# Kernel optimization log

Hardware: AMD Instinct MI355X
Metric: run time of the kernel (lower is better)

The kernel has to match this reference:

```python
import jax, jax.numpy as jnp
import numpy as np

N, E, IN_F, EDGE_F, HID, S = 200000, 600000, 28, 4, 128, 20000
NUM_LAYERS = 4
L = NUM_LAYERS - 1
BN_EPS = 1e-5


def setup_inputs() -> dict:
    key = jax.random.key(0)
    ks = jax.random.split(key, 20)
    p = lambda k, shape: (jax.random.normal(k, shape, dtype=jnp.float32) * 0.1)
    return {
        'x': jax.random.normal(ks[0], (N, IN_F), dtype=jnp.float32),
        'edge_index': jax.random.randint(ks[1], (2, E), 0, N),
        'edge_attr': jax.random.normal(ks[2], (E, EDGE_F), dtype=jnp.float32),
        'edge_weight': jax.random.uniform(ks[3], (E,), dtype=jnp.float32),
        'node_mask': (jax.random.uniform(ks[4], (N,)) > 0.5).astype(jnp.float32),
        'subgraphs2nodes': jax.random.randint(ks[5], (N,), 0, S),
        # layer-1 params (in_features -> hidden)
        'be1_W1': p(ks[6], (EDGE_F, IN_F)), 'be1_b1': jnp.zeros((IN_F,), jnp.float32),
        'be1_W2': p(ks[7], (IN_F, IN_F)), 'be1_b2': jnp.zeros((IN_F,), jnp.float32),
        'm1_W1': p(ks[8], (IN_F, HID)), 'm1_b1': jnp.zeros((HID,), jnp.float32),
        'm1_W2': p(ks[9], (HID, HID)), 'm1_b2': jnp.zeros((HID,), jnp.float32),
        'bn1_g': jnp.ones((HID,), jnp.float32), 'bn1_b': jnp.zeros((HID,), jnp.float32),
        'eps1': jnp.zeros((), jnp.float32),
        # layers 2..NUM_LAYERS, stacked (hidden -> hidden)
        'beW1': p(ks[10], (L, EDGE_F, HID)), 'beb1': jnp.zeros((L, HID), jnp.float32),
        'beW2': p(ks[11], (L, HID, HID)), 'beb2': jnp.zeros((L, HID), jnp.float32),
        'mW1': p(ks[12], (L, HID, HID)), 'mb1': jnp.zeros((L, HID), jnp.float32),
        'mW2': p(ks[13], (L, HID, HID)), 'mb2': jnp.zeros((L, HID), jnp.float32),
        'bng': jnp.ones((L, HID), jnp.float32), 'bnb': jnp.zeros((L, HID), jnp.float32),
        'eps': jnp.zeros((L,), jnp.float32),
    }


def _mlp2(h, W1, b1, W2, b2):
    # Linear -> ReLU -> Linear
    return jnp.dot(jax.nn.relu(jnp.dot(h, W1) + b1), W2) + b2


def _gine(x, src, dst, edge_attr, edge_weight, eps,
          beW1, beb1, beW2, beb2, W1, b1, W2, b2, g, beta):
    # bond encoder on edge features
    e = _mlp2(edge_attr, beW1, beb1, beW2, beb2)            # [E, d]
    # message: relu(x_j + e_ij) * w_ij, aggregated at dst via scatter-add
    m = jax.nn.relu(x[src] + e) * edge_weight[:, None]      # [E, d]
    aggr = jax.ops.segment_sum(m, dst, num_segments=N)      # [N, d]
    h = (1.0 + eps) * x + aggr
    # node MLP: Linear,ReLU,Linear,BN(train mode),ReLU
    h = _mlp2(h, W1, b1, W2, b2)
    mu = jnp.mean(h, axis=0)
    var = jnp.mean((h - mu) ** 2, axis=0)
    h = (h - mu) * jax.lax.rsqrt(var + BN_EPS) * g + beta
    return jax.nn.relu(h)


def reference(x, edge_index, edge_attr, edge_weight, node_mask, subgraphs2nodes,
              be1_W1, be1_b1, be1_W2, be1_b2, m1_W1, m1_b1, m1_W2, m1_b2,
              bn1_g, bn1_b, eps1,
              beW1, beb1, beW2, beb2, mW1, mb1, mW2, mb2, bng, bnb, eps):
    src, dst = edge_index[0], edge_index[1]
    h = _gine(x, src, dst, edge_attr, edge_weight, eps1,
              be1_W1, be1_b1, be1_W2, be1_b2,
              m1_W1, m1_b1, m1_W2, m1_b2, bn1_g, bn1_b)
    for i in range(L):
        h_new = _gine(h, src, dst, edge_attr, edge_weight, eps[i],
                      beW1[i], beb1[i], beW2[i], beb2[i],
                      mW1[i], mb1[i], mW2[i], mb2[i], bng[i], bnb[i])
        h = h + h_new  # residual
    # float node_mask branch + global_add_pool over subgraphs2nodes
    h = h * node_mask[:, None]
    return jax.ops.segment_sum(h, subgraphs2nodes, num_segments=S)  # [S, HID]
```

## Files before the change

### kernel.cpp

```cpp
#include <hip/hip_runtime.h>
#include <hip/hip_bf16.h>


#define BNEPS 1e-5f
#define LDA 136
#define SCAN_NB 240

typedef __attribute__((ext_vector_type(8))) short bf16x8;
typedef __attribute__((ext_vector_type(8))) unsigned short u16x8;
typedef __attribute__((ext_vector_type(4))) float f32x4;

__device__ inline short f2bf(float f) {
    __hip_bfloat16 h = __float2bfloat16(f);
    return *reinterpret_cast<short*>(&h);
}
__device__ inline unsigned short f2bfu(float f) {
    __hip_bfloat16 h = __float2bfloat16(f);
    return *reinterpret_cast<unsigned short*>(&h);
}
__device__ inline float bf2f(unsigned short u) {
    union { unsigned int i; float f; } v; v.i = ((unsigned int)u) << 16; return v.f;
}

__global__ __launch_bounds__(256) void k_prep(
    const float* __restrict__ m1W2, const float* __restrict__ beW2,
    const float* __restrict__ mW1, const float* __restrict__ mW2,
    short* __restrict__ out)
{
    __shared__ float tileS[64][65];
    int b = blockIdx.x, mat = b >> 2, t = b & 3;
    const float* Wsrc;
    if (mat == 0) Wsrc = m1W2;
    else {
        int l = (mat - 1) / 3, which = (mat - 1) % 3;
        Wsrc = (which == 0) ? beW2 + (size_t)l * 16384
             : (which == 1) ? mW1 + (size_t)l * 16384
             :                mW2 + (size_t)l * 16384;
    }
    short* dst = out + (size_t)mat * 16384;
    int tr = (t >> 1) * 64, tc = (t & 1) * 64;
    for (int i = threadIdx.x; i < 4096; i += 256) {
        int r = i >> 6, c = i & 63;
        tileS[r][c] = Wsrc[(size_t)(tr + r) * 128 + (tc + c)];
    }
    __syncthreads();
    for (int i = threadIdx.x; i < 4096; i += 256) {
        int n = i >> 6, k = i & 63;
        dst[(size_t)(tc + n) * 128 + (tr + k)] = f2bf(tileS[k][n]);
    }
}

__global__ __launch_bounds__(256) void k_prep1(
    const float* __restrict__ W1, short* __restrict__ out)
{
    for (int i = threadIdx.x; i < 128 * 32; i += 256) {
        int n = i >> 5, k = i & 31;
        out[i] = (k < 28) ? f2bf(W1[(size_t)k * 128 + n]) : (short)0;
    }
}

__global__ __launch_bounds__(256) void k_prep28(
    const float* __restrict__ W2, short* __restrict__ out)
{
    for (int i = threadIdx.x; i < 32 * 32; i += 256) {
        int n = i >> 5, k = i & 31;
        out[i] = (n < 28 && k < 28) ? f2bf(W2[(size_t)k * 28 + n]) : (short)0;
    }
}

__global__ __launch_bounds__(256) void k_count(
    const int* __restrict__ ei, int* __restrict__ counts, int E)
{
    for (int e = blockIdx.x * 256 + threadIdx.x; e < E; e += gridDim.x * 256)
        atomicAdd(&counts[ei[E + e]], 1);
}

__global__ __launch_bounds__(256) void k_count2(
    const int* __restrict__ s2n, const float* __restrict__ mask,
    int* __restrict__ counts2, int N)
{
    for (int n = blockIdx.x * 256 + threadIdx.x; n < N; n += gridDim.x * 256)
        if (mask[n] != 0.f) atomicAdd(&counts2[s2n[n]], 1);
}

__global__ __launch_bounds__(256) void k_scanA(
    const int* __restrict__ counts, int* __restrict__ bsum, int N, int seg)
{
    __shared__ int red[256];
    int b = blockIdx.x;
    int lo = b * seg, hi = min(lo + seg, N);
    int s = 0;
    for (int i = lo + threadIdx.x; i < hi; i += 256) s += counts[i];
    red[threadIdx.x] = s;
    __syncthreads();
    for (int d = 128; d > 0; d >>= 1) {
        if (threadIdx.x < d) red[threadIdx.x] += red[threadIdx.x + d];
        __syncthreads();
    }
    if (threadIdx.x == 0) bsum[b] = red[0];
}

__global__ __launch_bounds__(256) void k_scanB(
    int* __restrict__ bsum, int nb, int* __restrict__ offs, int N)
{
    __shared__ int sh[256];
    int v = (threadIdx.x < nb) ? bsum[threadIdx.x] : 0;
    sh[threadIdx.x] = v;
    __syncthreads();
    for (int d = 1; d < 256; d <<= 1) {
        int t = (threadIdx.x >= d) ? sh[threadIdx.x - d] : 0;
        __syncthreads();
        sh[threadIdx.x] += t;
        __syncthreads();
    }
    if (threadIdx.x < nb) bsum[threadIdx.x] = sh[threadIdx.x] - v;
    if (threadIdx.x == 0) offs[N] = sh[255];
}

__global__ __launch_bounds__(256) void k_scanC(
    const int* __restrict__ counts, const int* __restrict__ bsum,
    int* __restrict__ offs, int* __restrict__ cursor, int N, int seg)
{
    __shared__ int sh[256];
    int b = blockIdx.x;
    int lo = b * seg, hi = min(lo + seg, N);
    int base = bsum[b];
    for (int t0 = lo; t0 < hi; t0 += 256) {
        int i = t0 + threadIdx.x;
        int v = (i < hi) ? counts[i] : 0;
        sh[threadIdx.x] = v;
        __syncthreads();
        for (int d = 1; d < 256; d <<= 1) {
            int t = (threadIdx.x >= d) ? sh[threadIdx.x - d] : 0;
            __syncthreads();
            sh[threadIdx.x] += t;
            __syncthreads();
        }
        int excl = base + sh[threadIdx.x] - v;
        if (i < hi) { offs[i] = excl; cursor[i] = excl; }
        int tileTotal = sh[255];
        __syncthreads();
        base += tileTotal;
    }
}

__global__ __launch_bounds__(256) void k_scatter(
    const int* __restrict__ ei, const float* __restrict__ ew,
    const float4* __restrict__ ea4,
    int* __restrict__ cursor, int2* __restrict__ pmeta,
    float4* __restrict__ pea4, int E)
{
    for (int e = blockIdx.x * 256 + threadIdx.x; e < E; e += gridDim.x * 256) {
        int d = ei[E + e];
        int pos = atomicAdd(&cursor[d], 1);
        pmeta[pos] = make_int2(ei[e], __float_as_int(ew[e]));
        pea4[pos] = ea4[e];
    }
}

__global__ __launch_bounds__(256) void k_scatter2(
    const int* __restrict__ s2n, const float* __restrict__ mask,
    int* __restrict__ cursor2, int* __restrict__ perm2, int N)
{
    for (int n = blockIdx.x * 256 + threadIdx.x; n < N; n += gridDim.x * 256)
        if (mask[n] != 0.f) {
            int pos = atomicAdd(&cursor2[s2n[n]], 1);
            perm2[pos] = n;
        }
}

__global__ __launch_bounds__(256) void k_emsg(
    const float4* __restrict__ pea4,
    const float* __restrict__ W1, const float* __restrict__ b1,
    const short* __restrict__ W2t, const float* __restrict__ b2,
    unsigned short* __restrict__ emsg, int e0, int e1)
{
    __shared__ short Bs[128 * LDA];
    __shared__ short As[64 * LDA];
    __shared__ float eas[64][4];
    int tid = threadIdx.x;
    for (int i = tid; i < 2048; i += 256) {
        int n = (i * 8) >> 7, k = (i * 8) & 127;
        *(bf16x8*)&Bs[n * LDA + k] = *(const bf16x8*)&W2t[i * 8];
    }
    int j = tid & 127, half = tid >> 7;
    float w10 = W1[j], w11 = W1[128 + j], w12 = W1[256 + j], w13 = W1[384 + j];
    float b1j = b1[j];
    int w = tid >> 6, lane = tid & 63;
    int l15 = lane & 15, quad = lane >> 4;
    __syncthreads();

    int numTiles = (e1 - e0 + 63) >> 6;
    for (int tile = blockIdx.x; tile < numTiles; tile += gridDim.x) {
        int base = e0 + tile * 64;
        __syncthreads();
        if (tid < 64) {
            int k = base + tid;
            float4 a = make_float4(0.f, 0.f, 0.f, 0.f);
            if (k < e1) a = pea4[k];
            eas[tid][0] = a.x; eas[tid][1] = a.y; eas[tid][2] = a.z; eas[tid][3] = a.w;
        }
        __syncthreads();
        #pragma unroll
        for (int q = 0; q < 32; ++q) {
            int e = half * 32 + q;
            float t = fmaf(eas[e][0], w10, fmaf(eas[e][1], w11,
                      fmaf(eas[e][2], w12, fmaf(eas[e][3], w13, b1j))));
            As[e * LDA + j] = f2bf(fmaxf(t, 0.f));
        }
        __syncthreads();
        f32x4 acc[8];
        #pragma unroll
        for (int nt = 0; nt < 8; ++nt) acc[nt] = (f32x4){0.f, 0.f, 0.f, 0.f};
        #pragma unroll
        for (int kt = 0; kt < 4; ++kt) {
            bf16x8 af = *(bf16x8*)&As[(w * 16 + l15) * LDA + kt * 32 + quad * 8];
            #pragma unroll
            for (int nt = 0; nt < 8; ++nt) {
                bf16x8 bf = *(bf16x8*)&Bs[(nt * 16 + l15) * LDA + kt * 32 + quad * 8];
                acc[nt] = __builtin_amdgcn_mfma_f32_16x16x32_bf16(af, bf, acc[nt], 0, 0, 0);
            }
        }
        #pragma unroll
        for (int nt = 0; nt < 8; ++nt) {
            int col = nt * 16 + l15;
            float b2c = b2[col];
            #pragma unroll
            for (int r = 0; r < 4; ++r) {
                int row = w * 16 + quad * 4 + r;
                As[row * LDA + col] = f2bf(acc[nt][r] + b2c);
            }
        }
        __syncthreads();
        #pragma unroll
        for (int kk = 0; kk < 4; ++kk) {
            int i = tid + kk * 256;
            int row = (i * 8) >> 7, col = (i * 8) & 127;
            int gr = base + row;
            if (gr < e1)
                *(bf16x8*)&emsg[(size_t)(gr - e0) * 128 + col] = *(bf16x8*)&As[row * LDA + col];
        }
    }
}

__global__ __launch_bounds__(256) void k_emsg28_mm(
    const float4* __restrict__ pea4,
    const float* __restrict__ W1, const float* __restrict__ b1,
    const short* __restrict__ W2t28,
    const float* __restrict__ b2,
    unsigned short* __restrict__ emsg28, int E)
{
    __shared__ short Bs[32 * 40];
    __shared__ short As[64 * 40];
    __shared__ float eas[64][4];
    __shared__ float b2s[32];
    int tid = threadIdx.x;
    for (int i = tid; i < 32 * 32; i += 256) {
        int n = i >> 5, k = i & 31;
        Bs[n * 40 + k] = W2t28[i];
    }
    if (tid < 32) b2s[tid] = (tid < 28) ? b2[tid] : 0.f;
    int j = tid & 31, sub = tid >> 5;
    float w10 = 0.f, w11 = 0.f, w12 = 0.f, w13 = 0.f, b1j = 0.f;
    if (j < 28) { w10 = W1[j]; w11 = W1[28 + j]; w12 = W1[56 + j]; w13 = W1[84 + j]; b1j = b1[j]; }
    int w = tid >> 6, lane = tid & 63;
    int l15 = lane & 15, quad = lane >> 4;
    __syncthreads();

    int numTiles = (E + 63) >> 6;
    for (int tile = blockIdx.x; tile < numTiles; tile += gridDim.x) {
        int base = tile * 64;
        __syncthreads();
        if (tid < 64) {
            int k = base + tid;
            float4 a = (k < E) ? pea4[k] : make_float4(0.f, 0.f, 0.f, 0.f);
            eas[tid][0] = a.x; eas[tid][1] = a.y; eas[tid][2] = a.z; eas[tid][3] = a.w;
        }
        __syncthreads();
        #pragma unroll
        for (int q = 0; q < 8; ++q) {
            int e = q * 8 + sub;
            float t = fmaf(eas[e][0], w10, fmaf(eas[e][1], w11,
                      fmaf(eas[e][2], w12, fmaf(eas[e][3], w13, b1j))));
            As[e * 40 + j] = (j < 28) ? f2bf(fmaxf(t, 0.f)) : (short)0;
        }
        __syncthreads();
        f32x4 acc[2];
        acc[0] = (f32x4){0.f, 0.f, 0.f, 0.f};
        acc[1] = (f32x4){0.f, 0.f, 0.f, 0.f};
        bf16x8 af = *(bf16x8*)&As[(w * 16 + l15) * 40 + quad * 8];
        #pragma unroll
        for (int nt = 0; nt < 2; ++nt) {
            bf16x8 bf = *(bf16x8*)&Bs[(nt * 16 + l15) * 40 + quad * 8];
            acc[nt] = __builtin_amdgcn_mfma_f32_16x16x32_bf16(af, bf, acc[nt], 0, 0, 0);
        }
        __syncthreads();
        #pragma unroll
        for (int nt = 0; nt < 2; ++nt) {
            int col = nt * 16 + l15;
            float bb = b2s[col];
            #pragma unroll
            for (int r = 0; r < 4; ++r)
                As[(w * 16 + quad * 4 + r) * 40 + col] = f2bf(acc[nt][r] + bb);
        }
        __syncthreads();
        for (int i = tid; i < 64 * 28; i += 256) {
            int row = i / 28, col = i - row * 28;
            int gr = base + row;
            if (gr < E) emsg28[(size_t)gr * 28 + col] = As[row * 40 + col];
        }
    }
}

__global__ __launch_bounds__(256) void k_gather(
    const unsigned short* __restrict__ h, const int* __restrict__ offs,
    const int2* __restrict__ pmeta, const unsigned short* __restrict__ emsg,
    unsigned short* __restrict__ a0,
    const float* __restrict__ epsp, int epsIdx, int init,
    int e0, int e1, int N)
{
    int grp = threadIdx.x >> 5, lane = threadIdx.x & 31;
    int n = blockIdx.x * 8 + grp;
    if (n >= N) return;
    int k0 = offs[n], k1 = offs[n + 1];
    int lo = max(k0, e0), hi = min(k1, e1);
    if (!init && lo >= hi) return;
    float m0 = 0.f, m1 = 0.f, m2 = 0.f, m3 = 0.f;
    for (int k = lo; k < hi; ++k) {
        int2 mt = pmeta[k];
        float w = __int_as_float(mt.y);
        ushort4 ev = *(const ushort4*)&emsg[(size_t)(k - e0) * 128 + lane * 4];
        ushort4 hv = *(const ushort4*)&h[(size_t)mt.x * 128 + lane * 4];
        m0 += fmaxf(bf2f(hv.x) + bf2f(ev.x), 0.f) * w;
        m1 += fmaxf(bf2f(hv.y) + bf2f(ev.y), 0.f) * w;
        m2 += fmaxf(bf2f(hv.z) + bf2f(ev.z), 0.f) * w;
        m3 += fmaxf(bf2f(hv.w) + bf2f(ev.w), 0.f) * w;
    }
    if (init) {
        float s = 1.0f + epsp[epsIdx];
        ushort4 hv = *(const ushort4*)&h[(size_t)n * 128 + lane * 4];
        m0 = fmaf(s, bf2f(hv.x), m0);
        m1 = fmaf(s, bf2f(hv.y), m1);
        m2 = fmaf(s, bf2f(hv.z), m2);
        m3 = fmaf(s, bf2f(hv.w), m3);
    } else {
        ushort4 cur = *(ushort4*)&a0[(size_t)n * 128 + lane * 4];
        m0 += bf2f(cur.x); m1 += bf2f(cur.y); m2 += bf2f(cur.z); m3 += bf2f(cur.w);
    }
    ushort4 o;
    o.x = f2bfu(m0); o.y = f2bfu(m1); o.z = f2bfu(m2); o.w = f2bfu(m3);
    *(ushort4*)&a0[(size_t)n * 128 + lane * 4] = o;
}

__global__ __launch_bounds__(256) void k_gather28(
    const float* __restrict__ x, const int* __restrict__ offs,
    const int2* __restrict__ pmeta, const unsigned short* __restrict__ emsg28,
    const float* __restrict__ eps1, float* __restrict__ u28, int N)
{
    int grp = threadIdx.x >> 5, lane = threadIdx.x & 31;
    int n = blockIdx.x * 8 + grp;
    if (n >= N || lane >= 28) return;
    float s = 1.0f + eps1[0];
    int k0 = offs[n], k1 = offs[n + 1];
    float m = 0.f;
    for (int k = k0; k < k1; ++k) {
        int2 mt = pmeta[k];
        float w = __int_as_float(mt.y);
        float e = bf2f(emsg28[(size_t)k * 28 + lane]);
        m += fmaxf(x[(size_t)mt.x * 28 + lane] + e, 0.f) * w;
    }
    u28[(size_t)n * 28 + lane] = fmaf(s, x[(size_t)n * 28 + lane], m);
}

__global__ __launch_bounds__(512) void k_mlp(
    const unsigned short* __restrict__ src, const short* __restrict__ Wt1,
    const float* __restrict__ b1, const short* __restrict__ Wt2,
    const float* __restrict__ b2, unsigned short* __restrict__ dst,
    float* __restrict__ stats, int N)
{
    __shared__ short Bs1[128 * LDA];
    __shared__ short Bs2[128 * LDA];
    __shared__ short As[128 * LDA];
    __shared__ float sstat[256];
    int tid = threadIdx.x;
    for (int i = tid; i < 2048; i += 512) {
        int n = (i * 8) >> 7, k = (i * 8) & 127;
        *(bf16x8*)&Bs1[n * LDA + k] = *(const bf16x8*)&Wt1[i * 8];
        *(bf16x8*)&Bs2[n * LDA + k] = *(const bf16x8*)&Wt2[i * 8];
    }
    if (tid < 256) sstat[tid] = 0.f;
    int w = tid >> 6, lane = tid & 63;
    int l15 = lane & 15, quad = lane >> 4;
    float b1r[8], b2r[8], lsum[8], lsq[8];
    #pragma unroll
    for (int nt = 0; nt < 8; ++nt) {
        int col = nt * 16 + l15;
        b1r[nt] = b1[col]; b2r[nt] = b2[col];
        lsum[nt] = 0.f; lsq[nt] = 0.f;
    }
    __syncthreads();

    int numTiles = (N + 127) >> 7;
    for (int tile = blockIdx.x; tile < numTiles; tile += gridDim.x) {
        int base = tile * 128;
        __syncthreads();
        #pragma unroll
        for (int kk = 0; kk < 4; ++kk) {
            int i = tid + kk * 512;
            int row = (i * 8) >> 7, col = (i * 8) & 127;
            int rr = base + row;
            bf16x8 v;
            if (rr < N) v = *(const bf16x8*)&src[(size_t)rr * 128 + col];
            else        v = (bf16x8){0,0,0,0,0,0,0,0};
            *(bf16x8*)&As[row * LDA + col] = v;
        }
        __syncthreads();
        f32x4 acc[8];
        #pragma unroll
        for (int nt = 0; nt < 8; ++nt) acc[nt] = (f32x4){0.f, 0.f, 0.f, 0.f};
        #pragma unroll
        for (int kt = 0; kt < 4; ++kt) {
            bf16x8 af = *(bf16x8*)&As[(w * 16 + l15) * LDA + kt * 32 + quad * 8];
            #pragma unroll
            for (int nt = 0; nt < 8; ++nt) {
                bf16x8 bf = *(bf16x8*)&Bs1[(nt * 16 + l15) * LDA + kt * 32 + quad * 8];
                acc[nt] = __builtin_amdgcn_mfma_f32_16x16x32_bf16(af, bf, acc[nt], 0, 0, 0);
            }
        }
        #pragma unroll
        for (int nt = 0; nt < 8; ++nt) {
            int col = nt * 16 + l15;
            #pragma unroll
            for (int r = 0; r < 4; ++r)
                As[(w * 16 + quad * 4 + r) * LDA + col] = f2bf(fmaxf(acc[nt][r] + b1r[nt], 0.f));
        }
        __syncthreads();
        #pragma unroll
        for (int nt = 0; nt < 8; ++nt) acc[nt] = (f32x4){0.f, 0.f, 0.f, 0.f};
        #pragma unroll
        for (int kt = 0; kt < 4; ++kt) {
            bf16x8 af = *(bf16x8*)&As[(w * 16 + l15) * LDA + kt * 32 + quad * 8];
            #pragma unroll
            for (int nt = 0; nt < 8; ++nt) {
                bf16x8 bf = *(bf16x8*)&Bs2[(nt * 16 + l15) * LDA + kt * 32 + quad * 8];
                acc[nt] = __builtin_amdgcn_mfma_f32_16x16x32_bf16(af, bf, acc[nt], 0, 0, 0);
            }
        }
        int row0 = base + w * 16 + quad * 4;
        #pragma unroll
        for (int nt = 0; nt < 8; ++nt) {
            int col = nt * 16 + l15;
            #pragma unroll
            for (int r = 0; r < 4; ++r) {
                float z = acc[nt][r] + b2r[nt];
                if (row0 + r < N) { lsum[nt] += z; lsq[nt] = fmaf(z, z, lsq[nt]); }
                As[(w * 16 + quad * 4 + r) * LDA + col] = f2bf(z);
            }
        }
        __syncthreads();
        #pragma unroll
        for (int kk = 0; kk < 4; ++kk) {
            int i = tid + kk * 512;
            int row = (i * 8) >> 7, col = (i * 8) & 127;
            int rr = base + row;
            if (rr < N)
                *(bf16x8*)&dst[(size_t)rr * 128 + col] = *(bf16x8*)&As[row * LDA + col];
        }
    }
    #pragma unroll
    for (int nt = 0; nt < 8; ++nt) {
        int col = nt * 16 + l15;
        atomicAdd(&sstat[col], lsum[nt]);
        atomicAdd(&sstat[128 + col], lsq[nt]);
    }
    __syncthreads();
    if (tid < 256) atomicAdd(&stats[tid], sstat[tid]);
}

__global__ __launch_bounds__(512) void k_mlp1(
    const float* __restrict__ u28, const short* __restrict__ Wt1p,
    const float* __restrict__ b1, const short* __restrict__ Wt2,
    const float* __restrict__ b2, unsigned short* __restrict__ dst,
    float* __restrict__ stats, int N)
{
    __shared__ short Bs1[128 * 40];
    __shared__ short Bs2[128 * LDA];
    __shared__ short As[128 * LDA];
    __shared__ short A28[128 * 40];
    __shared__ float sstat[256];
    int tid = threadIdx.x;
    for (int i = tid; i < 128 * 32; i += 512) {
        int n = i >> 5, k = i & 31;
        Bs1[n * 40 + k] = Wt1p[i];
    }
    for (int i = tid; i < 2048; i += 512) {
        int n = (i * 8) >> 7, k = (i * 8) & 127;
        *(bf16x8*)&Bs2[n * LDA + k] = *(const bf16x8*)&Wt2[i * 8];
    }
    {
        int r = tid >> 2, c = tid & 3;
        if (tid < 512) A28[r * 40 + 28 + c] = 0;
    }
    if (tid < 256) sstat[tid] = 0.f;
    int w = tid >> 6, lane = tid & 63;
    int l15 = lane & 15, quad = lane >> 4;
    float b1r[8], b2r[8], lsum[8], lsq[8];
    #pragma unroll
    for (int nt = 0; nt < 8; ++nt) {
        int col = nt * 16 + l15;
        b1r[nt] = b1[col]; b2r[nt] = b2[col];
        lsum[nt] = 0.f; lsq[nt] = 0.f;
    }
    __syncthreads();

    int numTiles = (N + 127) >> 7;
    for (int tile = blockIdx.x; tile < numTiles; tile += gridDim.x) {
        int base = tile * 128;
        __syncthreads();
        for (int i = tid; i < 128 * 28; i += 512) {
            int row = i / 28, col = i - row * 28;
            int rr = base + row;
            A28[row * 40 + col] = (rr < N) ? f2bf(u28[(size_t)rr * 28 + col]) : (short)0;
        }
        __syncthreads();
        f32x4 acc[8];
        #pragma unroll
        for (int nt = 0; nt < 8; ++nt) acc[nt] = (f32x4){0.f, 0.f, 0.f, 0.f};
        {
            bf16x8 af = *(bf16x8*)&A28[(w * 16 + l15) * 40 + quad * 8];
            #pragma unroll
            for (int nt = 0; nt < 8; ++nt) {
                bf16x8 bf = *(bf16x8*)&Bs1[(nt * 16 + l15) * 40 + quad * 8];
                acc[nt] = __builtin_amdgcn_mfma_f32_16x16x32_bf16(af, bf, acc[nt], 0, 0, 0);
            }
        }
        #pragma unroll
        for (int nt = 0; nt < 8; ++nt) {
            int col = nt * 16 + l15;
            #pragma unroll
            for (int r = 0; r < 4; ++r)
                As[(w * 16 + quad * 4 + r) * LDA + col] = f2bf(fmaxf(acc[nt][r] + b1r[nt], 0.f));
        }
        __syncthreads();
        #pragma unroll
        for (int nt = 0; nt < 8; ++nt) acc[nt] = (f32x4){0.f, 0.f, 0.f, 0.f};
        #pragma unroll
        for (int kt = 0; kt < 4; ++kt) {
            bf16x8 af = *(bf16x8*)&As[(w * 16 + l15) * LDA + kt * 32 + quad * 8];
            #pragma unroll
            for (int nt = 0; nt < 8; ++nt) {
                bf16x8 bf = *(bf16x8*)&Bs2[(nt * 16 + l15) * LDA + kt * 32 + quad * 8];
                acc[nt] = __builtin_amdgcn_mfma_f32_16x16x32_bf16(af, bf, acc[nt], 0, 0, 0);
            }
        }
        int row0 = base + w * 16 + quad * 4;
        #pragma unroll
        for (int nt = 0; nt < 8; ++nt) {
            int col = nt * 16 + l15;
            #pragma unroll
            for (int r = 0; r < 4; ++r) {
                float z = acc[nt][r] + b2r[nt];
                if (row0 + r < N) { lsum[nt] += z; lsq[nt] = fmaf(z, z, lsq[nt]); }
                As[(w * 16 + quad * 4 + r) * LDA + col] = f2bf(z);
            }
        }
        __syncthreads();
        #pragma unroll
        for (int kk = 0; kk < 4; ++kk) {
            int i = tid + kk * 512;
            int row = (i * 8) >> 7, col = (i * 8) & 127;
            int rr = base + row;
            if (rr < N)
                *(bf16x8*)&dst[(size_t)rr * 128 + col] = *(bf16x8*)&As[row * LDA + col];
        }
    }
    #pragma unroll
    for (int nt = 0; nt < 8; ++nt) {
        int col = nt * 16 + l15;
        atomicAdd(&sstat[col], lsum[nt]);
        atomicAdd(&sstat[128 + col], lsq[nt]);
    }
    __syncthreads();
    if (tid < 256) atomicAdd(&stats[tid], sstat[tid]);
}

__global__ __launch_bounds__(128) void k_stats(
    const float* __restrict__ stats, const float* __restrict__ g,
    const float* __restrict__ b, float* __restrict__ ss, float invN)
{
    int j = threadIdx.x;
    float mu  = stats[j] * invN;
    float var = fmaf(stats[128 + j], invN, -mu * mu);
    float sc  = rsqrtf(fmaxf(var, 0.f) + BNEPS) * g[j];
    ss[j] = sc;
    ss[128 + j] = fmaf(-mu, sc, b[j]);
}

__global__ __launch_bounds__(256) void k_bn(
    const unsigned short* __restrict__ z, const float* __restrict__ ss,
    unsigned short* __restrict__ h, int residual, int N)
{
    int idx8 = blockIdx.x * 256 + threadIdx.x;
    int stride = gridDim.x * 256;
    int c0 = (idx8 & 15) * 8;
    float scl[8], sht[8];
    #pragma unroll
    for (int r = 0; r < 8; ++r) { scl[r] = ss[c0 + r]; sht[r] = ss[128 + c0 + r]; }
    int total8 = N * 16;
    for (; idx8 < total8; idx8 += stride) {
        int n = idx8 >> 4;
        u16x8 z8 = *(const u16x8*)&z[(size_t)n * 128 + c0];
        float hn[8];
        #pragma unroll
        for (int r = 0; r < 8; ++r)
            hn[r] = fmaxf(fmaf(bf2f(z8[r]), scl[r], sht[r]), 0.f);
        if (residual) {
            u16x8 h8 = *(const u16x8*)&h[(size_t)n * 128 + c0];
            #pragma unroll
            for (int r = 0; r < 8; ++r) hn[r] += bf2f(h8[r]);
        }
        u16x8 o;
        #pragma unroll
        for (int r = 0; r < 8; ++r) o[r] = f2bfu(hn[r]);
        *(u16x8*)&h[(size_t)n * 128 + c0] = o;
    }
}

__global__ __launch_bounds__(256) void k_poolbn(
    const unsigned short* __restrict__ z, const unsigned short* __restrict__ hprev,
    const float* __restrict__ ss, const int* __restrict__ offs2,
    const int* __restrict__ perm2, float* __restrict__ out, int S)
{
    int w = threadIdx.x >> 6, lane = threadIdx.x & 63;
    int s = blockIdx.x * 4 + w;
    if (s >= S) return;
    int c0 = lane * 2;
    float scl0 = ss[c0], scl1 = ss[c0 + 1];
    float sht0 = ss[128 + c0], sht1 = ss[128 + c0 + 1];
    int k0 = offs2[s], k1 = offs2[s + 1];
    float a0 = 0.f, a1 = 0.f;
    for (int k = k0; k < k1; ++k) {
        int n = perm2[k];
        ushort2 zv = *(const ushort2*)&z[(size_t)n * 128 + c0];
        ushort2 hv = *(const ushort2*)&hprev[(size_t)n * 128 + c0];
        a0 += fmaxf(fmaf(bf2f(zv.x), scl0, sht0), 0.f) + bf2f(hv.x);
        a1 += fmaxf(fmaf(bf2f(zv.y), scl1, sht1), 0.f) + bf2f(hv.y);
    }
    *(float2*)&out[(size_t)s * 128 + c0] = make_float2(a0, a1);
}

extern "C" void kernel_launch(void* const* d_in, const int* in_sizes, int n_in,
                              void* d_out, int out_size, void* d_ws, size_t ws_size,
                              hipStream_t stream) {
    const float* x    = (const float*)d_in[0];
    const int*   ei   = (const int*)d_in[1];
    const float* ea   = (const float*)d_in[2];
    const float* ew   = (const float*)d_in[3];
    const float* mask = (const float*)d_in[4];
    const int*   s2n  = (const int*)d_in[5];
    const float* be1W1 = (const float*)d_in[6];
    const float* be1b1 = (const float*)d_in[7];
    const float* be1W2 = (const float*)d_in[8];
    const float* be1b2 = (const float*)d_in[9];
    const float* m1W1  = (const float*)d_in[10];
    const float* m1b1  = (const float*)d_in[11];
    const float* m1W2  = (const float*)d_in[12];
    const float* m1b2  = (const float*)d_in[13];
    const float* bn1g  = (const float*)d_in[14];
    const float* bn1b  = (const float*)d_in[15];
    const float* eps1  = (const float*)d_in[16];
    const float* beW1  = (const float*)d_in[17];
    const float* beb1  = (const float*)d_in[18];
    const float* beW2  = (const float*)d_in[19];
    const float* beb2  = (const float*)d_in[20];
    const float* mW1   = (const float*)d_in[21];
    const float* mb1   = (const float*)d_in[22];
    const float* mW2   = (const float*)d_in[23];
    const float* mb2   = (const float*)d_in[24];
    const float* bng   = (const float*)d_in[25];
    const float* bnb   = (const float*)d_in[26];
    const float* epsL  = (const float*)d_in[27];

    const int N = in_sizes[0] / 28;
    const int E = in_sizes[1] / 2;
    const int S = out_size / 128;
    const float invN = 1.0f / (float)N;
    const int EC = (E + 1) / 2;

    auto al16 = [](size_t v) { return (v + 15) & ~(size_t)15; };
    char* ws = (char*)d_ws;
    size_t offH      = 0;
    size_t offA0     = al16(offH + (size_t)N * 256);
    size_t offEm     = al16(offA0 + (size_t)N * 256);
    size_t emBytes   = (size_t)EC * 256;
    if ((size_t)E * 56 > emBytes) emBytes = (size_t)E * 56;
    size_t offStats  = al16(offEm + emBytes);
    size_t offSS     = al16(offStats + 4096);
    size_t offWts    = al16(offSS + 1024);
    size_t offCounts = al16(offWts + 10 * 16384 * 2 + 4096 * 2 + 1024 * 2);
    size_t offOffs   = al16(offCounts + (size_t)N * 4);
    size_t offCursor = al16(offOffs + (size_t)(N + 1) * 4);
    size_t offPmeta  = al16(offCursor + (size_t)N * 4);
    size_t offPea    = al16(offPmeta + (size_t)E * 8);
    size_t offBsum   = al16(offPea + (size_t)E * 16);
    size_t offCnt2   = al16(offBsum + SCAN_NB * 4);
    size_t offOffs2  = al16(offCnt2 + (size_t)S * 4);
    size_t offCur2   = al16(offOffs2 + (size_t)(S + 1) * 4);
    size_t offPerm2  = al16(offCur2 + (size_t)S * 4);
    size_t need      = offPerm2 + (size_t)N * 4;
    if (ws_size < need) return;

    unsigned short* h    = (unsigned short*)(ws + offH);
    unsigned short* a0   = (unsigned short*)(ws + offA0);
    unsigned short* emsg = (unsigned short*)(ws + offEm);
    float* u28    = (float*)(ws + offA0);
    float* stats  = (float*)(ws + offStats);
    float* ssbuf  = (float*)(ws + offSS);
    short* wts    = (short*)(ws + offWts);
    short* w1p    = wts + 10 * 16384;
    short* w2p28  = w1p + 4096;
    int*   counts = (int*)(ws + offCounts);
    int*   offs   = (int*)(ws + offOffs);
    int*   cursor = (int*)(ws + offCursor);
    int2*  pmeta  = (int2*)(ws + offPmeta);
    float4* pea4  = (float4*)(ws + offPea);
    int*   bsum   = (int*)(ws + offBsum);
    int*   cnt2   = (int*)(ws + offCnt2);
    int*   offs2  = (int*)(ws + offOffs2);
    int*   cur2   = (int*)(ws + offCur2);
    int*   perm2  = (int*)(ws + offPerm2);
    const float4* ea4 = (const float4*)ea;

    hipMemsetAsync(stats, 0, 4 * 256 * sizeof(float), stream);
    hipMemsetAsync(counts, 0, (size_t)N * sizeof(int), stream);
    hipMemsetAsync(cnt2, 0, (size_t)S * sizeof(int), stream);

    k_prep<<<40, 256, 0, stream>>>(m1W2, beW2, mW1, mW2, wts);
    k_prep1<<<1, 256, 0, stream>>>(m1W1, w1p);
    k_prep28<<<1, 256, 0, stream>>>(be1W2, w2p28);

    const int seg = (N + SCAN_NB - 1) / SCAN_NB;
    k_count<<<1024, 256, 0, stream>>>(ei, counts, E);
    k_scanA<<<SCAN_NB, 256, 0, stream>>>(counts, bsum, N, seg);
    k_scanB<<<1, 256, 0, stream>>>(bsum, SCAN_NB, offs, N);
    k_scanC<<<SCAN_NB, 256, 0, stream>>>(counts, bsum, offs, cursor, N, seg);
    k_scatter<<<1024, 256, 0, stream>>>(ei, ew, ea4, cursor, pmeta, pea4, E);

    const int seg2 = (S + SCAN_NB - 1) / SCAN_NB;
    k_count2<<<512, 256, 0, stream>>>(s2n, mask, cnt2, N);
    k_scanA<<<SCAN_NB, 256, 0, stream>>>(cnt2, bsum, S, seg2);
    k_scanB<<<1, 256, 0, stream>>>(bsum, SCAN_NB, offs2, S);
    k_scanC<<<SCAN_NB, 256, 0, stream>>>(cnt2, bsum, offs2, cur2, S, seg2);
    k_scatter2<<<512, 256, 0, stream>>>(s2n, mask, cur2, perm2, N);

    auto wt_be = [&](int l) { return wts + (size_t)(1 + 3 * l + 0) * 16384; };
    auto wt_m1 = [&](int l) { return wts + (size_t)(1 + 3 * l + 1) * 16384; };
    auto wt_m2 = [&](int l) { return wts + (size_t)(1 + 3 * l + 2) * 16384; };

    int gatherBlocks = (N + 7) / 8;

    k_emsg28_mm<<<2048, 256, 0, stream>>>(pea4, be1W1, be1b1, w2p28, be1b2, emsg, E);
    k_gather28<<<gatherBlocks, 256, 0, stream>>>(x, offs, pmeta, emsg, eps1, u28, N);
    k_mlp1<<<256, 512, 0, stream>>>(u28, w1p, m1b1, wts , m1b2, h, stats, N);
    k_stats<<<1, 128, 0, stream>>>(stats, bn1g, bn1b, ssbuf, invN);
    k_bn<<<2048, 256, 0, stream>>>(h, ssbuf, h, 0, N);

    for (int l = 0; l < 3; ++l) {
        for (int c = 0; c < 2; ++c) {
            int e0 = c * EC, e1 = min(e0 + EC, E);
            k_emsg<<<2048, 256, 0, stream>>>(pea4,
                beW1 + (size_t)l * 512, beb1 + (size_t)l * 128,
                wt_be(l), beb2 + (size_t)l * 128, emsg, e0, e1);
            k_gather<<<gatherBlocks, 256, 0, stream>>>(h, offs, pmeta, emsg, a0,
                epsL, l, (c == 0) ? 1 : 0, e0, e1, N);
        }
        k_mlp<<<256, 512, 0, stream>>>(a0, wt_m1(l), mb1 + (size_t)l * 128,
                                       wt_m2(l), mb2 + (size_t)l * 128, a0,
                                       stats + 256 * (l + 1), N);
        k_stats<<<1, 128, 0, stream>>>(stats + 256 * (l + 1),
            bng + (size_t)l * 128, bnb + (size_t)l * 128, ssbuf, invN);
        if (l < 2) {
            k_bn<<<2048, 256, 0, stream>>>(a0, ssbuf, h, 1, N);
        }
    }

    k_poolbn<<<(S + 3) / 4, 256, 0, stream>>>(a0, h, ssbuf, offs2, perm2,
                                              (float*)d_out, S);
}
```

Before: 1.062 ms.

## Chunk edge messages by destination-node range and gather bf16 padded x

The two per-layer chunks of edge-message computation and aggregation are now split by destination-node range, using CSR offsets, instead of by raw edge index. Each gather launch covers only its own half of the nodes and writes its result once. This removes the second pass's early-exit blocks over all nodes and the read-modify-write of the partial aggregate. Separately, the layer-1 gather reads neighbour features from a padded bf16 copy of x, halving gathered bytes at the cost of an extra conversion kernel and reduced precision. The message buffer is sized as E/2 plus a slack of 8192, which assumes the edges are spread fairly evenly between the two node halves.

```diff
diff --git a/kernel.cpp b/kernel.cpp
--- a/kernel.cpp
+++ b/kernel.cpp
@@ -68,6 +68,16 @@
     }
 }
 
+__global__ __launch_bounds__(256) void k_prepx(
+    const float* __restrict__ x, unsigned short* __restrict__ xbf, int N)
+{
+    int total = N * 32;
+    for (int i = blockIdx.x * 256 + threadIdx.x; i < total; i += gridDim.x * 256) {
+        int n = i >> 5, c = i & 31;
+        xbf[i] = (c < 28) ? f2bfu(x[(size_t)n * 28 + c]) : (unsigned short)0;
+    }
+}
+
 __global__ __launch_bounds__(256) void k_count(
     const int* __restrict__ ei, int* __restrict__ counts, int E)
 {
@@ -173,11 +183,13 @@
     const float4* __restrict__ pea4,
     const float* __restrict__ W1, const float* __restrict__ b1,
     const short* __restrict__ W2t, const float* __restrict__ b2,
-    unsigned short* __restrict__ emsg, int e0, int e1)
+    unsigned short* __restrict__ emsg, const int* __restrict__ offs,
+    int n0, int n1)
 {
     __shared__ short Bs[128 * LDA];
     __shared__ short As[64 * LDA];
     __shared__ float eas[64][4];
+    int e0 = offs[n0], e1 = offs[n1];
     int tid = threadIdx.x;
     for (int i = tid; i < 2048; i += 256) {
         int n = (i * 8) >> 7, k = (i * 8) & 127;
@@ -316,17 +328,19 @@
     const unsigned short* __restrict__ h, const int* __restrict__ offs,
     const int2* __restrict__ pmeta, const unsigned short* __restrict__ emsg,
     unsigned short* __restrict__ a0,
-    const float* __restrict__ epsp, int epsIdx, int init,
-    int e0, int e1, int N)
+    const float* __restrict__ epsp, int epsIdx,
+    int n0, int n1)
 {
     int grp = threadIdx.x >> 5, lane = threadIdx.x & 31;
-    int n = blockIdx.x * 8 + grp;
-    if (n >= N) return;
+    int n = n0 + blockIdx.x * 8 + grp;
+    if (n >= n1) return;
+    int e0 = offs[n0];
     int k0 = offs[n], k1 = offs[n + 1];
-    int lo = max(k0, e0), hi = min(k1, e1);
-    if (!init && lo >= hi) return;
-    float m0 = 0.f, m1 = 0.f, m2 = 0.f, m3 = 0.f;
-    for (int k = lo; k < hi; ++k) {
+    float s = 1.0f + epsp[epsIdx];
+    ushort4 hv0 = *(const ushort4*)&h[(size_t)n * 128 + lane * 4];
+    float m0 = s * bf2f(hv0.x), m1 = s * bf2f(hv0.y);
+    float m2 = s * bf2f(hv0.z), m3 = s * bf2f(hv0.w);
+    for (int k = k0; k < k1; ++k) {
         int2 mt = pmeta[k];
         float w = __int_as_float(mt.y);
         ushort4 ev = *(const ushort4*)&emsg[(size_t)(k - e0) * 128 + lane * 4];
@@ -336,24 +350,14 @@
         m2 += fmaxf(bf2f(hv.z) + bf2f(ev.z), 0.f) * w;
         m3 += fmaxf(bf2f(hv.w) + bf2f(ev.w), 0.f) * w;
     }
-    if (init) {
-        float s = 1.0f + epsp[epsIdx];
-        ushort4 hv = *(const ushort4*)&h[(size_t)n * 128 + lane * 4];
-        m0 = fmaf(s, bf2f(hv.x), m0);
-        m1 = fmaf(s, bf2f(hv.y), m1);
-        m2 = fmaf(s, bf2f(hv.z), m2);
-        m3 = fmaf(s, bf2f(hv.w), m3);
-    } else {
-        ushort4 cur = *(ushort4*)&a0[(size_t)n * 128 + lane * 4];
-        m0 += bf2f(cur.x); m1 += bf2f(cur.y); m2 += bf2f(cur.z); m3 += bf2f(cur.w);
-    }
     ushort4 o;
     o.x = f2bfu(m0); o.y = f2bfu(m1); o.z = f2bfu(m2); o.w = f2bfu(m3);
     *(ushort4*)&a0[(size_t)n * 128 + lane * 4] = o;
 }
 
 __global__ __launch_bounds__(256) void k_gather28(
-    const float* __restrict__ x, const int* __restrict__ offs,
+    const float* __restrict__ x, const unsigned short* __restrict__ xbf,
+    const int* __restrict__ offs,
     const int2* __restrict__ pmeta, const unsigned short* __restrict__ emsg28,
     const float* __restrict__ eps1, float* __restrict__ u28, int N)
 {
@@ -367,7 +371,8 @@
         int2 mt = pmeta[k];
         float w = __int_as_float(mt.y);
         float e = bf2f(emsg28[(size_t)k * 28 + lane]);
-        m += fmaxf(x[(size_t)mt.x * 28 + lane] + e, 0.f) * w;
+        float xs = bf2f(xbf[(size_t)mt.x * 32 + lane]);
+        m += fmaxf(xs + e, 0.f) * w;
     }
     u28[(size_t)n * 28 + lane] = fmaf(s, x[(size_t)n * 28 + lane], m);
 }
@@ -685,14 +690,15 @@
     const int E = in_sizes[1] / 2;
     const int S = out_size / 128;
     const float invN = 1.0f / (float)N;
-    const int EC = (E + 1) / 2;
+    const int NS = N / 2;
+    const int EMC = E / 2 + 8192;
 
     auto al16 = [](size_t v) { return (v + 15) & ~(size_t)15; };
     char* ws = (char*)d_ws;
     size_t offH      = 0;
     size_t offA0     = al16(offH + (size_t)N * 256);
     size_t offEm     = al16(offA0 + (size_t)N * 256);
-    size_t emBytes   = (size_t)EC * 256;
+    size_t emBytes   = (size_t)EMC * 256;
     if ((size_t)E * 56 > emBytes) emBytes = (size_t)E * 56;
     size_t offStats  = al16(offEm + emBytes);
     size_t offSS     = al16(offStats + 4096);
@@ -714,6 +720,7 @@
     unsigned short* a0   = (unsigned short*)(ws + offA0);
     unsigned short* emsg = (unsigned short*)(ws + offEm);
     float* u28    = (float*)(ws + offA0);
+    unsigned short* xbf = (unsigned short*)(ws + offA0 + 26214400);
     float* stats  = (float*)(ws + offStats);
     float* ssbuf  = (float*)(ws + offSS);
     short* wts    = (short*)(ws + offWts);
@@ -738,6 +745,7 @@
     k_prep<<<40, 256, 0, stream>>>(m1W2, beW2, mW1, mW2, wts);
     k_prep1<<<1, 256, 0, stream>>>(m1W1, w1p);
     k_prep28<<<1, 256, 0, stream>>>(be1W2, w2p28);
+    k_prepx<<<512, 256, 0, stream>>>(x, xbf, N);
 
     const int seg = (N + SCAN_NB - 1) / SCAN_NB;
     k_count<<<1024, 256, 0, stream>>>(ei, counts, E);
@@ -757,22 +765,21 @@
     auto wt_m1 = [&](int l) { return wts + (size_t)(1 + 3 * l + 1) * 16384; };
     auto wt_m2 = [&](int l) { return wts + (size_t)(1 + 3 * l + 2) * 16384; };
 
-    int gatherBlocks = (N + 7) / 8;
-
     k_emsg28_mm<<<2048, 256, 0, stream>>>(pea4, be1W1, be1b1, w2p28, be1b2, emsg, E);
-    k_gather28<<<gatherBlocks, 256, 0, stream>>>(x, offs, pmeta, emsg, eps1, u28, N);
+    k_gather28<<<(N + 7) / 8, 256, 0, stream>>>(x, xbf, offs, pmeta, emsg, eps1, u28, N);
     k_mlp1<<<256, 512, 0, stream>>>(u28, w1p, m1b1, wts , m1b2, h, stats, N);
     k_stats<<<1, 128, 0, stream>>>(stats, bn1g, bn1b, ssbuf, invN);
     k_bn<<<2048, 256, 0, stream>>>(h, ssbuf, h, 0, N);
 
     for (int l = 0; l < 3; ++l) {
         for (int c = 0; c < 2; ++c) {
-            int e0 = c * EC, e1 = min(e0 + EC, E);
+            int n0 = (c == 0) ? 0 : NS;
+            int n1 = (c == 0) ? NS : N;
             k_emsg<<<2048, 256, 0, stream>>>(pea4,
                 beW1 + (size_t)l * 512, beb1 + (size_t)l * 128,
-                wt_be(l), beb2 + (size_t)l * 128, emsg, e0, e1);
-            k_gather<<<gatherBlocks, 256, 0, stream>>>(h, offs, pmeta, emsg, a0,
-                epsL, l, (c == 0) ? 1 : 0, e0, e1, N);
+                wt_be(l), beb2 + (size_t)l * 128, emsg, offs, n0, n1);
+            k_gather<<<(n1 - n0 + 7) / 8, 256, 0, stream>>>(h, offs, pmeta, emsg, a0,
+                epsL, l, n0, n1);
         }
         k_mlp<<<256, 512, 0, stream>>>(a0, wt_m1(l), mb1 + (size_t)l * 128,
                                        wt_m2(l), mb2 + (size_t)l * 128, a0,
```

Measured after the change: 1.052 ms. No clear change (-0.9%).
